# Kernel tuning notes

Hardware: AMD Instinct MI355X
Metric: run time of the kernel (lower is better)

The kernel has to match this reference:

```python
import jax, jax.numpy as jnp
import numpy as np

B, V = 4, 10242
N = B * V            # 40968 packed vertices
E_PER = 30720        # edges per mesh
HID = 128


def _bilinear_sample(fm, grid):
    """pytorch3d vert_align core: grid_sample(align_corners=True, bilinear).
    fm: [B,C,H,W], grid: [B,V,2] xy in [-1,1] -> [B,V,C]."""
    b_, c_, h_, w_ = fm.shape
    x = (grid[..., 0] + 1.0) * 0.5 * (w_ - 1)
    y = (grid[..., 1] + 1.0) * 0.5 * (h_ - 1)
    x0f, y0f = jnp.floor(x), jnp.floor(y)
    wx1, wy1 = x - x0f, y - y0f
    wx0, wy0 = 1.0 - wx1, 1.0 - wy1
    x0 = jnp.clip(x0f, 0, w_ - 1).astype(jnp.int32)
    x1 = jnp.clip(x0f + 1, 0, w_ - 1).astype(jnp.int32)
    y0 = jnp.clip(y0f, 0, h_ - 1).astype(jnp.int32)
    y1 = jnp.clip(y0f + 1, 0, h_ - 1).astype(jnp.int32)
    fmt = jnp.transpose(fm, (0, 2, 3, 1))  # [B,H,W,C]
    bi = jnp.arange(b_)[:, None]
    g = lambda yy, xx: fmt[bi, yy, xx]     # [B,V,C]
    return ((wy0 * wx0)[..., None] * g(y0, x0)
            + (wy0 * wx1)[..., None] * g(y0, x1)
            + (wy1 * wx0)[..., None] * g(y1, x0)
            + (wy1 * wx1)[..., None] * g(y1, x1))


def _graph_conv(x, edges, w0, b0, w1, b1):
    """pytorch3d GraphConv (undirected): W0 x_i + sum over both edge dirs of W1 x_j."""
    h0 = x @ w0 + b0
    h1 = x @ w1 + b1
    e0, e1 = edges[:, 0], edges[:, 1]
    agg = jnp.zeros_like(h0).at[e0].add(h1[e1]).at[e1].add(h1[e0])
    return h0 + agg


def setup_inputs() -> dict:
    key = jax.random.key(0)
    ks = jax.random.split(key, 20)
    s = 0.05
    # per-mesh edges, offset into packed index space
    e = jax.random.randint(ks[0], (B, E_PER, 2), 0, V)
    e = e + (jnp.arange(B) * V)[:, None, None]
    return {
        "feat1": jax.random.normal(ks[1], (B, 256, 56, 56), jnp.float32),
        "feat2": jax.random.normal(ks[2], (B, 512, 28, 28), jnp.float32),
        "feat3": jax.random.normal(ks[3], (B, 1024, 14, 14), jnp.float32),
        "feat4": jax.random.normal(ks[4], (B, 2048, 7, 7), jnp.float32),
        "aligned_verts": jax.random.uniform(ks[5], (B, V, 3), jnp.float32, -1.0, 1.0),
        "verts_packed": jax.random.normal(ks[6], (N, 3), jnp.float32),
        "image_enc": jax.random.normal(ks[7], (B, 256), jnp.float32),
        "edges": e.reshape(B * E_PER, 2).astype(jnp.int64),
        "bottleneck_w": jax.random.normal(ks[8], (3840, HID), jnp.float32) * s,
        "bottleneck_b": jnp.zeros((HID,), jnp.float32),
        "g0_w0": jax.random.normal(ks[9], (387, HID), jnp.float32) * s,
        "g0_b0": jnp.zeros((HID,), jnp.float32),
        "g0_w1": jax.random.normal(ks[10], (387, HID), jnp.float32) * s,
        "g0_b1": jnp.zeros((HID,), jnp.float32),
        "gw0": jax.random.normal(ks[11], (7, HID, HID), jnp.float32) * s,
        "gb0": jnp.zeros((7, HID), jnp.float32),
        "gw1": jax.random.normal(ks[12], (7, HID, HID), jnp.float32) * s,
        "gb1": jnp.zeros((7, HID), jnp.float32),
        "off_w": jax.random.normal(ks[13], (HID, 3), jnp.float32) * s,
        "off_b": jnp.zeros((3,), jnp.float32),
    }


def reference(feat1, feat2, feat3, feat4, aligned_verts, verts_packed, image_enc,
              edges, bottleneck_w, bottleneck_b, g0_w0, g0_b0, g0_w1, g0_b1,
              gw0, gb0, gw1, gb1, off_w, off_b):
    grid = aligned_verts[..., :2]  # vert_align uses xy only
    samp = jnp.concatenate([_bilinear_sample(f, grid)
                            for f in (feat1, feat2, feat3, feat4)], axis=-1)
    samp = samp.reshape(N, 3840)  # return_packed=True
    vfeat = jax.nn.relu(samp @ bottleneck_w + bottleneck_b)
    enc = jnp.repeat(image_enc, V, axis=0)  # repeat_interleave
    x = jnp.concatenate([vfeat, verts_packed, enc], axis=1)  # [N,387]
    x = jax.nn.relu(_graph_conv(x, edges, g0_w0, g0_b0, g0_w1, g0_b1))
    for i in range(7):
        x = jax.nn.relu(_graph_conv(x, edges, gw0[i], gb0[i], gw1[i], gb1[i]))
    return x @ off_w + off_b  # delta_v [N,3]
```

## Files before the change

kernel.cpp:

```cpp
#include <hip/hip_runtime.h>

static inline int ceil_div(int a, int b) { return (a + b - 1) / b; }

typedef __attribute__((ext_vector_type(8))) short short8;
typedef __attribute__((ext_vector_type(4))) float floatx4;

__device__ __forceinline__ unsigned short f2bf(float f) {
    unsigned int u = __float_as_uint(f);
    unsigned int r = (u + 0x7fffu + ((u >> 16) & 1u)) >> 16;
    return (unsigned short)r;
}
__device__ __forceinline__ float bf2f(unsigned short h) {
    return __uint_as_float(((unsigned int)h) << 16);
}

__global__ __launch_bounds__(1024) void scan1_k(const int* __restrict__ deg,
                                                int* __restrict__ excl,
                                                int* __restrict__ bsum, int Nv) {
    __shared__ int s[1024];
    int tid = threadIdx.x;
    int i = blockIdx.x * 1024 + tid;
    int v = (i < Nv) ? deg[i] : 0;
    s[tid] = v;
    __syncthreads();
    for (int off = 1; off < 1024; off <<= 1) {
        int t = (tid >= off) ? s[tid - off] : 0;
        __syncthreads();
        if (tid >= off) s[tid] += t;
        __syncthreads();
    }
    if (i < Nv) excl[i] = s[tid] - v;
    if (tid == 1023) bsum[blockIdx.x] = s[1023];
}

__global__ __launch_bounds__(64) void scan2_k(int* __restrict__ bsum, int nb) {
    __shared__ int s[64];
    int tid = threadIdx.x;
    int v = (tid < nb) ? bsum[tid] : 0;
    s[tid] = v;
    __syncthreads();
    for (int off = 1; off < 64; off <<= 1) {
        int t = (tid >= off) ? s[tid - off] : 0;
        __syncthreads();
        if (tid >= off) s[tid] += t;
        __syncthreads();
    }
    if (tid < nb) bsum[tid] = s[tid] - v;
}

__global__ __launch_bounds__(1024) void scan3_k(const int* __restrict__ excl,
                                                const int* __restrict__ bsum,
                                                const int* __restrict__ deg,
                                                int* __restrict__ rowptr,
                                                int* __restrict__ cursor, int Nv) {
    int i = blockIdx.x * 1024 + threadIdx.x;
    if (i < Nv) {
        int val = excl[i] + bsum[blockIdx.x];
        rowptr[i] = val;
        cursor[i] = val;
        if (i == Nv - 1) rowptr[Nv] = val + deg[i];
    }
}

__global__ __launch_bounds__(256) void fill_adj_k(const int* __restrict__ edges,
                                                  int* __restrict__ cursor,
                                                  int* __restrict__ adj, int E) {
    int e = blockIdx.x * blockDim.x + threadIdx.x;
    if (e < E) {
        int a = edges[2 * e], b = edges[2 * e + 1];
        adj[atomicAdd(&cursor[a], 1)] = b;
        adj[atomicAdd(&cursor[b], 1)] = a;
    }
}

__global__ __launch_bounds__(256) void fatpre_k(const int* __restrict__ edges,
                                                int* __restrict__ deg, int E, int nE,
                                                const float* __restrict__ g0w0,
                                                const float* __restrict__ g0w1,
                                                const float* __restrict__ gw0,
                                                const float* __restrict__ gw1,
                                                unsigned short* __restrict__ Wt,
                                                const float* __restrict__ enc,
                                                float* __restrict__ encp, int B_) {
    int bid = blockIdx.x;
    int tid = threadIdx.x;
    if (bid < nE) {
        int e = bid * 256 + tid;
        if (e < E) {
            atomicAdd(&deg[edges[2 * e]], 1);
            atomicAdd(&deg[edges[2 * e + 1]], 1);
        }
    } else if (bid < nE + 16) {
        int lh = bid - nE;
        int l = lh >> 1, h = lh & 1;
        const float* src;
        if (l == 0) src = h ? g0w1 : g0w0;
        else src = (h ? gw1 : gw0) + (size_t)(l - 1) * 16384;
        unsigned short* dst = Wt + (size_t)lh * 16384;
        for (int idx = tid; idx < 16384; idx += 256) {
            int n = idx >> 7, k = idx & 127;
            dst[n * 128 + k] = f2bf(src[k * 128 + n]);
        }
    } else {
        int b = bid - nE - 16;
        int sH = tid >> 7;
        int j = tid & 127;
        const float* w = sH ? g0w1 : g0w0;
        const float* eb = enc + b * 256;
        float acc = 0.f;
        for (int c = 0; c < 256; ++c) acc = fmaf(eb[c], w[(131 + c) * 128 + j], acc);
        encp[(sH * B_ + b) * 128 + j] = acc;
    }
}

__global__ __launch_bounds__(256) void proj_all_k(
    const float* __restrict__ fm1, const float* __restrict__ fm2,
    const float* __restrict__ fm3, const float* __restrict__ fm4,
    const float* __restrict__ bw, float* __restrict__ q1, float* __restrict__ q2,
    float* __restrict__ q3, float* __restrict__ q4, int B_) {
    __shared__ float Xs[32][64];
    __shared__ float Ws[32][128];
    int tid = threadIdx.x;

    int n1 = 49 * B_ * 4, n2 = 13 * B_ * 8, n3 = 4 * B_ * 16;
    int bid = blockIdx.x;
    const float* fm;
    const float* W;
    float* op;
    int C, HW, PT, idx;
    if (bid < n1) {
        fm = fm1; W = bw; op = q1; C = 256; HW = 3136; PT = 49; idx = bid;
    } else if (bid < n1 + n2) {
        fm = fm2; W = bw + 256 * 128; op = q2; C = 512; HW = 784; PT = 13; idx = bid - n1;
    } else if (bid < n1 + n2 + n3) {
        fm = fm3; W = bw + 768 * 128; op = q3; C = 1024; HW = 196; PT = 4; idx = bid - n1 - n2;
    } else {
        fm = fm4; W = bw + 1792 * 128; op = q4; C = 2048; HW = 49; PT = 1;
        idx = bid - n1 - n2 - n3;
    }
    int pt = idx % PT;
    int r2 = idx / PT;
    int b = r2 % B_;
    int zz = r2 / B_;
    int p0 = pt * 64;
    int c0 = zz * 64;
    int S = B_ * HW * 128;
    const float* fmb = fm + (size_t)b * C * HW;

    float acc[8][4];
#pragma unroll
    for (int i = 0; i < 8; i++)
#pragma unroll
        for (int j = 0; j < 4; j++) acc[i][j] = 0.f;

    bool vec_ok = ((HW & 3) == 0);
    for (int kc = c0; kc < c0 + 64; kc += 32) {
        {
            int p4 = (tid & 15) * 4;
            int k0 = tid >> 4;
#pragma unroll
            for (int kk = 0; kk < 32; kk += 16) {
                int k = k0 + kk;
                const float* src = fmb + (size_t)(kc + k) * HW + p0 + p4;
                float4 v;
                if (vec_ok && (p0 + p4 + 3 < HW)) {
                    v = *(const float4*)src;
                } else {
                    v.x = (p0 + p4 + 0 < HW) ? src[0] : 0.f;
                    v.y = (p0 + p4 + 1 < HW) ? src[1] : 0.f;
                    v.z = (p0 + p4 + 2 < HW) ? src[2] : 0.f;
                    v.w = (p0 + p4 + 3 < HW) ? src[3] : 0.f;
                }
                *(float4*)&Xs[k][p4] = v;
            }
        }
        {
            int j4 = (tid & 31) * 4;
            int k0 = tid >> 5;
#pragma unroll
            for (int kk = 0; kk < 32; kk += 8) {
                int k = k0 + kk;
                *(float4*)&Ws[k][j4] = *(const float4*)(W + (size_t)(kc + k) * 128 + j4);
            }
        }
        __syncthreads();
        int rb = (tid >> 5) * 8;
        int cb = (tid & 31) * 4;
#pragma unroll 8
        for (int k = 0; k < 32; ++k) {
            float xr[8], wc[4];
#pragma unroll
            for (int i = 0; i < 8; i++) xr[i] = Xs[k][rb + i];
#pragma unroll
            for (int j = 0; j < 4; j++) wc[j] = Ws[k][cb + j];
#pragma unroll
            for (int i = 0; i < 8; i++)
#pragma unroll
                for (int j = 0; j < 4; j++) acc[i][j] = fmaf(xr[i], wc[j], acc[i][j]);
        }
        __syncthreads();
    }
    int rb = (tid >> 5) * 8;
    int cb = (tid & 31) * 4;
    float* obase = op + (size_t)zz * S;
#pragma unroll
    for (int i = 0; i < 8; i++) {
        int p = p0 + rb + i;
        if (p < HW) {
            *(float4*)(obase + ((size_t)b * HW + p) * 128 + cb) =
                make_float4(acc[i][0], acc[i][1], acc[i][2], acc[i][3]);
        }
    }
}

__global__ __launch_bounds__(256) void reduce4_k(const float* __restrict__ q1,
                                                 const float* __restrict__ q2,
                                                 const float* __restrict__ q3,
                                                 const float* __restrict__ q4,
                                                 float* __restrict__ o1, float* __restrict__ o2,
                                                 float* __restrict__ o3, float* __restrict__ o4,
                                                 int S1, int S2, int S3, int S4) {
    int i = (blockIdx.x * 256 + threadIdx.x) * 4;
    const float* src;
    float* dst;
    int S, z, base;
    if (i < S1) {
        src = q1; dst = o1; S = S1; z = 4; base = i;
    } else if (i < S1 + S2) {
        src = q2; dst = o2; S = S2; z = 8; base = i - S1;
    } else if (i < S1 + S2 + S3) {
        src = q3; dst = o3; S = S3; z = 16; base = i - S1 - S2;
    } else if (i < S1 + S2 + S3 + S4) {
        src = q4; dst = o4; S = S4; z = 32; base = i - S1 - S2 - S3;
    } else {
        return;
    }
    float4 a = *(const float4*)(src + base);
    for (int zz = 1; zz < z; ++zz) {
        float4 b = *(const float4*)(src + (size_t)zz * S + base);
        a.x += b.x; a.y += b.y; a.z += b.z; a.w += b.w;
    }
    *(float4*)(dst + base) = a;
}

__device__ __forceinline__ float sample_level(const float* __restrict__ pp, int Hh, int Ww,
                                              float gx, float gy, int j) {
    float x = (gx + 1.f) * 0.5f * (float)(Ww - 1);
    float y = (gy + 1.f) * 0.5f * (float)(Hh - 1);
    float x0f = floorf(x), y0f = floorf(y);
    float wx1 = x - x0f, wy1 = y - y0f;
    float wx0 = 1.f - wx1, wy0 = 1.f - wy1;
    int x0 = (int)fminf(fmaxf(x0f, 0.f), (float)(Ww - 1));
    int x1 = (int)fminf(fmaxf(x0f + 1.f, 0.f), (float)(Ww - 1));
    int y0 = (int)fminf(fmaxf(y0f, 0.f), (float)(Hh - 1));
    int y1 = (int)fminf(fmaxf(y0f + 1.f, 0.f), (float)(Hh - 1));
    const float* r00 = pp + (size_t)(y0 * Ww + x0) * 128;
    const float* r01 = pp + (size_t)(y0 * Ww + x1) * 128;
    const float* r10 = pp + (size_t)(y1 * Ww + x0) * 128;
    const float* r11 = pp + (size_t)(y1 * Ww + x1) * 128;
    return wy0 * (wx0 * r00[j] + wx1 * r01[j]) + wy1 * (wx0 * r10[j] + wx1 * r11[j]);
}

__global__ __launch_bounds__(128) void sample_bottleneck_k(
    const float* __restrict__ av, const float* __restrict__ pp1, const float* __restrict__ pp2,
    const float* __restrict__ pp3, const float* __restrict__ pp4, const float* __restrict__ bb,
    const float* __restrict__ verts, const float* __restrict__ encp,
    const float* __restrict__ g0w0, const float* __restrict__ g0w1,
    const float* __restrict__ g0b0, const float* __restrict__ g0b1,
    unsigned short* __restrict__ X, unsigned short* __restrict__ H, int V_, int B_) {
    int n = blockIdx.x, j = threadIdx.x;
    int b = n / V_;
    float gx = av[(size_t)n * 3 + 0];
    float gy = av[(size_t)n * 3 + 1];
    float acc = bb[j];
    acc += sample_level(pp1 + (size_t)b * 3136 * 128, 56, 56, gx, gy, j);
    acc += sample_level(pp2 + (size_t)b * 784 * 128, 28, 28, gx, gy, j);
    acc += sample_level(pp3 + (size_t)b * 196 * 128, 14, 14, gx, gy, j);
    acc += sample_level(pp4 + (size_t)b * 49 * 128, 7, 7, gx, gy, j);
    X[(size_t)n * 128 + j] = f2bf(fmaxf(acc, 0.f));
    float v0 = verts[n * 3 + 0], v1 = verts[n * 3 + 1], v2 = verts[n * 3 + 2];
    float h0 = encp[(0 * B_ + b) * 128 + j] + g0b0[j] + v0 * g0w0[128 * 128 + j] +
               v1 * g0w0[129 * 128 + j] + v2 * g0w0[130 * 128 + j];
    float h1 = encp[(1 * B_ + b) * 128 + j] + g0b1[j] + v0 * g0w1[128 * 128 + j] +
               v1 * g0w1[129 * 128 + j] + v2 * g0w1[130 * 128 + j];
    H[(size_t)n * 256 + j] = f2bf(h0);
    H[(size_t)n * 256 + 128 + j] = f2bf(h1);
}

__global__ __launch_bounds__(256) void aggpre_k(const unsigned short* __restrict__ H,
                                                const int* __restrict__ rowptr,
                                                const int* __restrict__ adj,
                                                float* __restrict__ pre, int Nv) {
    int wave = threadIdx.x >> 6, lane = threadIdx.x & 63;
    int n = blockIdx.x * 4 + wave;
    if (n >= Nv) return;
    unsigned int u = *(const unsigned int*)(H + (size_t)n * 256 + 2 * lane);
    float a0 = bf2f((unsigned short)(u & 0xffff));
    float a1 = bf2f((unsigned short)(u >> 16));
    int s = rowptr[n], e = rowptr[n + 1];
    for (int t = s; t < e; t += 8) {
        int nb[8];
        unsigned int w[8];
#pragma unroll
        for (int q = 0; q < 8; ++q) {
            int idx = (t + q < e) ? (t + q) : (e - 1);
            nb[q] = adj[idx];
        }
#pragma unroll
        for (int q = 0; q < 8; ++q)
            w[q] = *(const unsigned int*)(H + (size_t)nb[q] * 256 + 128 + 2 * lane);
#pragma unroll
        for (int q = 0; q < 8; ++q) {
            if (t + q < e) {
                a0 += bf2f((unsigned short)(w[q] & 0xffff));
                a1 += bf2f((unsigned short)(w[q] >> 16));
            }
        }
    }
    pre[(size_t)n * 128 + 2 * lane] = a0;
    pre[(size_t)n * 128 + 2 * lane + 1] = a1;
}

__global__ __launch_bounds__(256) void agg_x_k(const unsigned short* __restrict__ X,
                                               const int* __restrict__ rowptr,
                                               const int* __restrict__ adj,
                                               unsigned short* __restrict__ Agg, int Nv) {
    int wave = threadIdx.x >> 6, lane = threadIdx.x & 63;
    int n = blockIdx.x * 4 + wave;
    if (n >= Nv) return;
    const unsigned int* Xu = (const unsigned int*)X;
    float a0 = 0.f, a1 = 0.f;
    int s = rowptr[n], e = rowptr[n + 1];
    for (int t = s; t < e; t += 8) {
        int nb[8];
        unsigned int w[8];
#pragma unroll
        for (int q = 0; q < 8; ++q) {
            int idx = (t + q < e) ? (t + q) : (e - 1);
            nb[q] = adj[idx];
        }
#pragma unroll
        for (int q = 0; q < 8; ++q) w[q] = Xu[(size_t)nb[q] * 64 + lane];
#pragma unroll
        for (int q = 0; q < 8; ++q) {
            if (t + q < e) {
                a0 += bf2f((unsigned short)(w[q] & 0xffff));
                a1 += bf2f((unsigned short)(w[q] >> 16));
            }
        }
    }
    unsigned int o = (unsigned int)f2bf(a0) | ((unsigned int)f2bf(a1) << 16);
    *(unsigned int*)(Agg + (size_t)n * 128 + 2 * lane) = o;
}

__global__ __launch_bounds__(256, 3) void gemm_dual_k(
    const unsigned short* __restrict__ Xin, const unsigned short* __restrict__ Agg,
    const unsigned short* __restrict__ Wt,
    const float* __restrict__ b0, const float* __restrict__ b1,
    const float* __restrict__ pre, const int* __restrict__ degv,
    unsigned short* __restrict__ Xout, int M) {
    __shared__ unsigned short wlds[16384];
    __shared__ unsigned short cs[64 * 72];
    __shared__ float bS[128];

    int tid = threadIdx.x;
    int m0 = blockIdx.x * 128;
    int yb = blockIdx.y;

    int wave = tid >> 6, lane = tid & 63;
    int row16 = lane & 15;
    int quad = lane >> 4;
    int wrow = wave * 16;

    short8 axT[2][4], agT[2][4];
    int dgT[2][4];
    {
        int g = min(m0 + wrow + row16, M - 1);
#pragma unroll
        for (int ks = 0; ks < 4; ++ks) {
            int koff = ks * 32 + quad * 8;
            axT[0][ks] = *(const short8*)(Xin + (size_t)g * 128 + koff);
            agT[0][ks] = *(const short8*)(Agg + (size_t)g * 128 + koff);
        }
#pragma unroll
        for (int rr = 0; rr < 4; ++rr)
            dgT[0][rr] = degv[min(m0 + wrow + quad * 4 + rr, M - 1)];
    }

    if (tid < 64) {
        bS[tid] = b0 ? b0[yb * 64 + tid] : 0.f;
        bS[64 + tid] = b1 ? b1[yb * 64 + tid] : 0.f;
    }

    const unsigned short* W0h = Wt + (size_t)yb * 64 * 128;
    const unsigned short* W1h = Wt + 16384 + (size_t)yb * 64 * 128;
#pragma unroll
    for (int l = 0; l < 8; ++l) {
        int idx = tid + l * 256;
        int half = idx >> 10;
        int r = (idx >> 4) & 63;
        int c16 = idx & 15;
        int sw = (c16 ^ (r & 15)) * 8;
        const unsigned short* src = (half ? W1h : W0h) + r * 128 + c16 * 8;
        *(short8*)&wlds[half * 8192 + r * 128 + sw] = *(const short8*)src;
    }
    __syncthreads();

    {
        int g = min(m0 + 64 + wrow + row16, M - 1);
#pragma unroll
        for (int ks = 0; ks < 4; ++ks) {
            int koff = ks * 32 + quad * 8;
            axT[1][ks] = *(const short8*)(Xin + (size_t)g * 128 + koff);
            agT[1][ks] = *(const short8*)(Agg + (size_t)g * 128 + koff);
        }
#pragma unroll
        for (int rr = 0; rr < 4; ++rr)
            dgT[1][rr] = degv[min(m0 + 64 + wrow + quad * 4 + rr, M - 1)];
    }

#pragma unroll
    for (int t = 0; t < 2; ++t) {
        int mT = m0 + t * 64;
        floatx4 acc[4];
#pragma unroll
        for (int j = 0; j < 4; j++) acc[j] = (floatx4){0.f, 0.f, 0.f, 0.f};

#pragma unroll
        for (int ks = 0; ks < 4; ++ks) {
            int c = ks * 4 + quad;
#pragma unroll
            for (int nt = 0; nt < 4; ++nt) {
                int wr = nt * 16 + row16;
                short8 bw0 = *(short8*)&wlds[wr * 128 + ((c ^ row16) * 8)];
                short8 bw1 = *(short8*)&wlds[8192 + wr * 128 + ((c ^ row16) * 8)];
                acc[nt] = __builtin_amdgcn_mfma_f32_16x16x32_bf16(axT[t][ks], bw0, acc[nt], 0, 0, 0);
                acc[nt] = __builtin_amdgcn_mfma_f32_16x16x32_bf16(agT[t][ks], bw1, acc[nt], 0, 0, 0);
            }
        }

#pragma unroll
        for (int nt = 0; nt < 4; ++nt) {
            int colh = nt * 16 + row16;
            int colg = yb * 64 + colh;
            float bc0 = bS[colh];
            float bc1 = bS[64 + colh];
#pragma unroll
            for (int rr = 0; rr < 4; ++rr) {
                int row = wrow + quad * 4 + rr;
                int gm = mT + row;
                float v = acc[nt][rr] + bc0 + (float)dgT[t][rr] * bc1;
                if (pre && gm < M) v += pre[(size_t)gm * 128 + colg];
                cs[row * 72 + colh] = f2bf(fmaxf(v, 0.f));
            }
        }
        __syncthreads();

        {
            int r = tid >> 2;
            int cq = (tid & 3) * 16;
            int gm = mT + r;
            if (gm < M) {
                unsigned short* dst = Xout + (size_t)gm * 128 + yb * 64 + cq;
                *(short8*)dst = *(short8*)&cs[r * 72 + cq];
                *(short8*)(dst + 8) = *(short8*)&cs[r * 72 + cq + 8];
            }
        }
        __syncthreads();
    }
}

__global__ __launch_bounds__(256) void head_k(const unsigned short* __restrict__ X,
                                              const float* __restrict__ off_w,
                                              const float* __restrict__ off_b,
                                              float* __restrict__ out, int Nv) {
    int wave = threadIdx.x >> 6, lane = threadIdx.x & 63;
    int n = blockIdx.x * 4 + wave;
    if (n >= Nv) return;
    unsigned int u = *(const unsigned int*)(X + (size_t)n * 128 + 2 * lane);
    float x0 = bf2f((unsigned short)(u & 0xffff));
    float x1 = bf2f((unsigned short)(u >> 16));
    int c0 = 2 * lane, c1 = 2 * lane + 1;
    float p0 = x0 * off_w[c0 * 3 + 0] + x1 * off_w[c1 * 3 + 0];
    float p1 = x0 * off_w[c0 * 3 + 1] + x1 * off_w[c1 * 3 + 1];
    float p2 = x0 * off_w[c0 * 3 + 2] + x1 * off_w[c1 * 3 + 2];
#pragma unroll
    for (int m = 1; m < 64; m <<= 1) {
        p0 += __shfl_xor(p0, m);
        p1 += __shfl_xor(p1, m);
        p2 += __shfl_xor(p2, m);
    }
    if (lane == 0) {
        out[n * 3 + 0] = p0 + off_b[0];
        out[n * 3 + 1] = p1 + off_b[1];
        out[n * 3 + 2] = p2 + off_b[2];
    }
}

extern "C" void kernel_launch(void* const* d_in, const int* in_sizes, int n_in, void* d_out,
                              int out_size, void* d_ws, size_t ws_size, hipStream_t stream) {
    const float* feat1 = (const float*)d_in[0];
    const float* feat2 = (const float*)d_in[1];
    const float* feat3 = (const float*)d_in[2];
    const float* feat4 = (const float*)d_in[3];
    const float* av = (const float*)d_in[4];
    const float* verts = (const float*)d_in[5];
    const float* image_enc = (const float*)d_in[6];
    const int* edges = (const int*)d_in[7];
    const float* bw = (const float*)d_in[8];
    const float* bb = (const float*)d_in[9];
    const float* g0w0 = (const float*)d_in[10];
    const float* g0b0 = (const float*)d_in[11];
    const float* g0w1 = (const float*)d_in[12];
    const float* g0b1 = (const float*)d_in[13];
    const float* gw0 = (const float*)d_in[14];
    const float* gb0 = (const float*)d_in[15];
    const float* gw1 = (const float*)d_in[16];
    const float* gb1 = (const float*)d_in[17];
    const float* off_w = (const float*)d_in[18];
    const float* off_b = (const float*)d_in[19];

    int B_ = in_sizes[6] / 256;
    int N_ = in_sizes[5] / 3;
    int V_ = N_ / B_;
    int E_ = in_sizes[7] / 2;

    char* wsb = (char*)d_ws;
    size_t off = 0;
    auto alloc = [&](size_t bytes) -> void* {
        void* p = (void*)(wsb + off);
        off += (bytes + 255) & ~(size_t)255;
        return p;
    };
    int S1 = B_ * 3136 * 128;
    int S2 = B_ * 784 * 128;
    int S3 = B_ * 196 * 128;
    int S4 = B_ * 49 * 128;
    float* pp1 = (float*)alloc((size_t)S1 * 4);
    float* pp2 = (float*)alloc((size_t)S2 * 4);
    float* pp3 = (float*)alloc((size_t)S3 * 4);
    float* pp4 = (float*)alloc((size_t)S4 * 4);
    float* q1 = (float*)alloc((size_t)4 * S1 * 4);
    float* q2 = (float*)alloc((size_t)8 * S2 * 4);
    float* q3 = (float*)alloc((size_t)16 * S3 * 4);
    float* q4 = (float*)alloc((size_t)32 * S4 * 4);
    unsigned short* XA = (unsigned short*)alloc((size_t)N_ * 128 * 2);
    unsigned short* XB = (unsigned short*)alloc((size_t)N_ * 128 * 2);
    unsigned short* AggB = (unsigned short*)alloc((size_t)N_ * 128 * 2);
    unsigned short* Hb = (unsigned short*)alloc((size_t)N_ * 256 * 2);
    float* pre = (float*)alloc((size_t)N_ * 128 * 4);
    unsigned short* Wt = (unsigned short*)alloc((size_t)8 * 2 * 128 * 128 * 2);
    float* encp = (float*)alloc((size_t)2 * B_ * 128 * 4);
    int* deg = (int*)alloc((size_t)(N_ + 1) * 4);
    int* rowptr = (int*)alloc((size_t)(N_ + 1) * 4);
    int* cursor = (int*)alloc((size_t)N_ * 4);
    int* excl = (int*)alloc((size_t)N_ * 4);
    int* bsum = (int*)alloc((size_t)64 * 4);
    int* adj = (int*)alloc((size_t)2 * E_ * 4);

    hipMemsetAsync(deg, 0, (N_ + 1) * sizeof(int), stream);

    int nE = ceil_div(E_, 256);
    fatpre_k<<<nE + 16 + B_, 256, 0, stream>>>(edges, deg, E_, nE, g0w0, g0w1, gw0, gw1, Wt,
                                               image_enc, encp, B_);

    int nb = ceil_div(N_, 1024);
    scan1_k<<<nb, 1024, 0, stream>>>(deg, excl, bsum, N_);
    scan2_k<<<1, 64, 0, stream>>>(bsum, nb);
    scan3_k<<<nb, 1024, 0, stream>>>(excl, bsum, deg, rowptr, cursor, N_);
    fill_adj_k<<<ceil_div(E_, 256), 256, 0, stream>>>(edges, cursor, adj, E_);

    int nproj = 49 * B_ * 4 + 13 * B_ * 8 + 4 * B_ * 16 + 1 * B_ * 32;
    proj_all_k<<<nproj, 256, 0, stream>>>(feat1, feat2, feat3, feat4, bw, q1, q2, q3, q4, B_);
    int tot4 = (S1 + S2 + S3 + S4) / 4;
    reduce4_k<<<ceil_div(tot4, 256), 256, 0, stream>>>(q1, q2, q3, q4, pp1, pp2, pp3, pp4, S1,
                                                       S2, S3, S4);

    sample_bottleneck_k<<<N_, 128, 0, stream>>>(av, pp1, pp2, pp3, pp4, bb, verts, encp, g0w0,
                                                g0w1, g0b0, g0b1, XA, Hb, V_, B_);

    aggpre_k<<<ceil_div(N_, 4), 256, 0, stream>>>(Hb, rowptr, adj, pre, N_);

    int agrid = ceil_div(N_, 4);
    dim3 ggrid(ceil_div(N_, 128), 2);
    agg_x_k<<<agrid, 256, 0, stream>>>(XA, rowptr, adj, AggB, N_);
    gemm_dual_k<<<ggrid, 256, 0, stream>>>(XA, AggB, Wt, nullptr, nullptr, pre, deg, XB, N_);
    unsigned short* Xc = XB;
    unsigned short* Xn = XA;
    for (int i = 0; i < 7; ++i) {
        agg_x_k<<<agrid, 256, 0, stream>>>(Xc, rowptr, adj, AggB, N_);
        gemm_dual_k<<<ggrid, 256, 0, stream>>>(Xc, AggB, Wt + (size_t)(i + 1) * 32768,
                                               gb0 + i * 128, gb1 + i * 128, nullptr, deg, Xn,
                                               N_);
        unsigned short* t = Xc;
        Xc = Xn;
        Xn = t;
    }
    head_k<<<ceil_div(N_, 4), 256, 0, stream>>>(Xc, off_w, off_b, (float*)d_out, N_);
}
```

Baseline: 493.5 us.

## Fuse neighbor aggregation into dual GEMM per graph-conv layer

Replaces the separate agg_x_k and gemm_dual_k launches with one kernel per layer. Each block gathers and sums neighbor features for 64 rows into LDS, using a wave-level CSR walk that flushes each row's sum when its edge range ends. It then runs both MFMA products over all 128 output columns using a 64KB LDS weight tile. This removes the Agg buffer round trip through global memory and half the launches. In exchange, LDS use per block is larger (occupancy hint drops to 2), and each wave walks its rows' edges serially, which can leave waves unevenly loaded.

```diff
diff --git a/kernel.cpp b/kernel.cpp
--- a/kernel.cpp
+++ b/kernel.cpp
@@ -321,152 +321,145 @@
     pre[(size_t)n * 128 + 2 * lane + 1] = a1;
 }
 
-__global__ __launch_bounds__(256) void agg_x_k(const unsigned short* __restrict__ X,
-                                               const int* __restrict__ rowptr,
-                                               const int* __restrict__ adj,
-                                               unsigned short* __restrict__ Agg, int Nv) {
-    int wave = threadIdx.x >> 6, lane = threadIdx.x & 63;
-    int n = blockIdx.x * 4 + wave;
-    if (n >= Nv) return;
-    const unsigned int* Xu = (const unsigned int*)X;
-    float a0 = 0.f, a1 = 0.f;
-    int s = rowptr[n], e = rowptr[n + 1];
-    for (int t = s; t < e; t += 8) {
-        int nb[8];
-        unsigned int w[8];
-#pragma unroll
-        for (int q = 0; q < 8; ++q) {
-            int idx = (t + q < e) ? (t + q) : (e - 1);
-            nb[q] = adj[idx];
-        }
-#pragma unroll
-        for (int q = 0; q < 8; ++q) w[q] = Xu[(size_t)nb[q] * 64 + lane];
-#pragma unroll
-        for (int q = 0; q < 8; ++q) {
-            if (t + q < e) {
-                a0 += bf2f((unsigned short)(w[q] & 0xffff));
-                a1 += bf2f((unsigned short)(w[q] >> 16));
-            }
-        }
-    }
-    unsigned int o = (unsigned int)f2bf(a0) | ((unsigned int)f2bf(a1) << 16);
-    *(unsigned int*)(Agg + (size_t)n * 128 + 2 * lane) = o;
-}
-
-__global__ __launch_bounds__(256, 3) void gemm_dual_k(
-    const unsigned short* __restrict__ Xin, const unsigned short* __restrict__ Agg,
+__global__ __launch_bounds__(256, 2) void layer_fused_k(
+    const unsigned short* __restrict__ Xin, const int* __restrict__ rowptr,
+    const int* __restrict__ adj,
     const unsigned short* __restrict__ Wt,
     const float* __restrict__ b0, const float* __restrict__ b1,
     const float* __restrict__ pre, const int* __restrict__ degv,
     unsigned short* __restrict__ Xout, int M) {
-    __shared__ unsigned short wlds[16384];
-    __shared__ unsigned short cs[64 * 72];
-    __shared__ float bS[128];
+    __shared__ unsigned short wlds[32768];
+    __shared__ unsigned short aggs[8192];
 
     int tid = threadIdx.x;
-    int m0 = blockIdx.x * 128;
-    int yb = blockIdx.y;
-
+    int m0 = blockIdx.x * 64;
     int wave = tid >> 6, lane = tid & 63;
     int row16 = lane & 15;
     int quad = lane >> 4;
-    int wrow = wave * 16;
-
-    short8 axT[2][4], agT[2][4];
-    int dgT[2][4];
+
+    int gbase = m0 + wave * 16;
+    int rend_l = rowptr[min(gbase + 1 + row16, M)];
+    int sW = rowptr[min(gbase, M)];
+    int eW = __shfl(rend_l, 15);
+
+    short8 axT[4];
     {
-        int g = min(m0 + wrow + row16, M - 1);
-#pragma unroll
-        for (int ks = 0; ks < 4; ++ks) {
-            int koff = ks * 32 + quad * 8;
-            axT[0][ks] = *(const short8*)(Xin + (size_t)g * 128 + koff);
-            agT[0][ks] = *(const short8*)(Agg + (size_t)g * 128 + koff);
-        }
-#pragma unroll
-        for (int rr = 0; rr < 4; ++rr)
-            dgT[0][rr] = degv[min(m0 + wrow + quad * 4 + rr, M - 1)];
-    }
-
-    if (tid < 64) {
-        bS[tid] = b0 ? b0[yb * 64 + tid] : 0.f;
-        bS[64 + tid] = b1 ? b1[yb * 64 + tid] : 0.f;
-    }
-
-    const unsigned short* W0h = Wt + (size_t)yb * 64 * 128;
-    const unsigned short* W1h = Wt + 16384 + (size_t)yb * 64 * 128;
-#pragma unroll
-    for (int l = 0; l < 8; ++l) {
+        int g = min(m0 + wave * 16 + row16, M - 1);
+#pragma unroll
+        for (int ks = 0; ks < 4; ++ks)
+            axT[ks] = *(const short8*)(Xin + (size_t)g * 128 + ks * 32 + quad * 8);
+    }
+    int dgT[4];
+#pragma unroll
+    for (int rr = 0; rr < 4; ++rr)
+        dgT[rr] = degv[min(m0 + wave * 16 + quad * 4 + rr, M - 1)];
+    float bc0[8], bc1[8];
+#pragma unroll
+    for (int nt = 0; nt < 8; ++nt) {
+        int colg = nt * 16 + row16;
+        bc0[nt] = b0 ? b0[colg] : 0.f;
+        bc1[nt] = b1 ? b1[colg] : 0.f;
+    }
+
+#pragma unroll
+    for (int l = 0; l < 16; ++l) {
         int idx = tid + l * 256;
-        int half = idx >> 10;
-        int r = (idx >> 4) & 63;
+        int half = idx >> 11;
+        int n = (idx >> 4) & 127;
         int c16 = idx & 15;
-        int sw = (c16 ^ (r & 15)) * 8;
-        const unsigned short* src = (half ? W1h : W0h) + r * 128 + c16 * 8;
-        *(short8*)&wlds[half * 8192 + r * 128 + sw] = *(const short8*)src;
+        int sw = (c16 ^ (n & 15)) * 8;
+        *(short8*)&wlds[half * 16384 + n * 128 + sw] =
+            *(const short8*)(Wt + (size_t)half * 16384 + n * 128 + c16 * 8);
+    }
+
+    {
+        const unsigned int* Xu = (const unsigned int*)Xin;
+        float a0 = 0.f, a1 = 0.f;
+        int r = 0;
+        int nextEnd = __shfl(rend_l, 0);
+        auto flush = [&](int rloc, float v0, float v1) {
+            unsigned int o = (unsigned int)f2bf(v0) | ((unsigned int)f2bf(v1) << 16);
+            *(unsigned int*)&aggs[(wave * 16 + rloc) * 128 + (((lane >> 2) ^ rloc) * 8) +
+                                  (lane & 3) * 2] = o;
+        };
+        for (int t = sW; t < eW; t += 8) {
+            int nb[8];
+            unsigned int w[8];
+#pragma unroll
+            for (int q = 0; q < 8; ++q) {
+                int idx = (t + q < eW) ? (t + q) : (eW - 1);
+                nb[q] = adj[idx];
+            }
+#pragma unroll
+            for (int q = 0; q < 8; ++q) w[q] = Xu[(size_t)nb[q] * 64 + lane];
+#pragma unroll
+            for (int q = 0; q < 8; ++q) {
+                int pos = t + q;
+                if (pos < eW) {
+                    while (pos >= nextEnd) {
+                        flush(r, a0, a1);
+                        a0 = 0.f;
+                        a1 = 0.f;
+                        ++r;
+                        nextEnd = __shfl(rend_l, r);
+                    }
+                    a0 += bf2f((unsigned short)(w[q] & 0xffff));
+                    a1 += bf2f((unsigned short)(w[q] >> 16));
+                }
+            }
+        }
+        while (r < 16) {
+            flush(r, a0, a1);
+            a0 = 0.f;
+            a1 = 0.f;
+            ++r;
+        }
     }
     __syncthreads();
 
+    floatx4 acc[8];
+#pragma unroll
+    for (int j = 0; j < 8; ++j) acc[j] = (floatx4){0.f, 0.f, 0.f, 0.f};
+#pragma unroll
+    for (int ks = 0; ks < 4; ++ks) {
+        int c = ks * 4 + quad;
+        short8 aAg = *(short8*)&aggs[(wave * 16 + row16) * 128 + ((c ^ row16) * 8)];
+#pragma unroll
+        for (int nt = 0; nt < 8; ++nt) {
+            int wr = nt * 16 + row16;
+            short8 bw0 = *(short8*)&wlds[wr * 128 + ((c ^ row16) * 8)];
+            short8 bw1 = *(short8*)&wlds[16384 + wr * 128 + ((c ^ row16) * 8)];
+            acc[nt] = __builtin_amdgcn_mfma_f32_16x16x32_bf16(axT[ks], bw0, acc[nt], 0, 0, 0);
+            acc[nt] = __builtin_amdgcn_mfma_f32_16x16x32_bf16(aAg, bw1, acc[nt], 0, 0, 0);
+        }
+    }
+
+#pragma unroll
+    for (int nt = 0; nt < 8; ++nt) {
+#pragma unroll
+        for (int rr = 0; rr < 4; ++rr) {
+            int row = wave * 16 + quad * 4 + rr;
+            int gm = m0 + row;
+            int colh = nt * 16 + row16;
+            float v = acc[nt][rr] + bc0[nt] + (float)dgT[rr] * bc1[nt];
+            if (pre && gm < M) v += pre[(size_t)gm * 128 + colh];
+            int ch = colh >> 3;
+            aggs[row * 128 + ((ch ^ (row & 15)) * 8) + (colh & 7)] = f2bf(fmaxf(v, 0.f));
+        }
+    }
+    __syncthreads();
+
     {
-        int g = min(m0 + 64 + wrow + row16, M - 1);
-#pragma unroll
-        for (int ks = 0; ks < 4; ++ks) {
-            int koff = ks * 32 + quad * 8;
-            axT[1][ks] = *(const short8*)(Xin + (size_t)g * 128 + koff);
-            agT[1][ks] = *(const short8*)(Agg + (size_t)g * 128 + koff);
-        }
-#pragma unroll
-        for (int rr = 0; rr < 4; ++rr)
-            dgT[1][rr] = degv[min(m0 + 64 + wrow + quad * 4 + rr, M - 1)];
-    }
-
-#pragma unroll
-    for (int t = 0; t < 2; ++t) {
-        int mT = m0 + t * 64;
-        floatx4 acc[4];
-#pragma unroll
-        for (int j = 0; j < 4; j++) acc[j] = (floatx4){0.f, 0.f, 0.f, 0.f};
-
-#pragma unroll
-        for (int ks = 0; ks < 4; ++ks) {
-            int c = ks * 4 + quad;
-#pragma unroll
-            for (int nt = 0; nt < 4; ++nt) {
-                int wr = nt * 16 + row16;
-                short8 bw0 = *(short8*)&wlds[wr * 128 + ((c ^ row16) * 8)];
-                short8 bw1 = *(short8*)&wlds[8192 + wr * 128 + ((c ^ row16) * 8)];
-                acc[nt] = __builtin_amdgcn_mfma_f32_16x16x32_bf16(axT[t][ks], bw0, acc[nt], 0, 0, 0);
-                acc[nt] = __builtin_amdgcn_mfma_f32_16x16x32_bf16(agT[t][ks], bw1, acc[nt], 0, 0, 0);
+        int r = tid >> 2;
+        int gm = m0 + r;
+        if (gm < M) {
+            unsigned short* dst = Xout + (size_t)gm * 128 + (tid & 3) * 32;
+#pragma unroll
+            for (int cc = 0; cc < 4; ++cc) {
+                int c = (tid & 3) * 4 + cc;
+                *(short8*)(dst + cc * 8) = *(short8*)&aggs[r * 128 + ((c ^ (r & 15)) * 8)];
             }
         }
-
-#pragma unroll
-        for (int nt = 0; nt < 4; ++nt) {
-            int colh = nt * 16 + row16;
-            int colg = yb * 64 + colh;
-            float bc0 = bS[colh];
-            float bc1 = bS[64 + colh];
-#pragma unroll
-            for (int rr = 0; rr < 4; ++rr) {
-                int row = wrow + quad * 4 + rr;
-                int gm = mT + row;
-                float v = acc[nt][rr] + bc0 + (float)dgT[t][rr] * bc1;
-                if (pre && gm < M) v += pre[(size_t)gm * 128 + colg];
-                cs[row * 72 + colh] = f2bf(fmaxf(v, 0.f));
-            }
-        }
-        __syncthreads();
-
-        {
-            int r = tid >> 2;
-            int cq = (tid & 3) * 16;
-            int gm = mT + r;
-            if (gm < M) {
-                unsigned short* dst = Xout + (size_t)gm * 128 + yb * 64 + cq;
-                *(short8*)dst = *(short8*)&cs[r * 72 + cq];
-                *(short8*)(dst + 8) = *(short8*)&cs[r * 72 + cq + 8];
-            }
-        }
-        __syncthreads();
     }
 }
 
@@ -546,7 +539,6 @@
     float* q4 = (float*)alloc((size_t)32 * S4 * 4);
     unsigned short* XA = (unsigned short*)alloc((size_t)N_ * 128 * 2);
     unsigned short* XB = (unsigned short*)alloc((size_t)N_ * 128 * 2);
-    unsigned short* AggB = (unsigned short*)alloc((size_t)N_ * 128 * 2);
     unsigned short* Hb = (unsigned short*)alloc((size_t)N_ * 256 * 2);
     float* pre = (float*)alloc((size_t)N_ * 128 * 4);
     unsigned short* Wt = (unsigned short*)alloc((size_t)8 * 2 * 128 * 128 * 2);
@@ -581,17 +573,15 @@
 
     aggpre_k<<<ceil_div(N_, 4), 256, 0, stream>>>(Hb, rowptr, adj, pre, N_);
 
-    int agrid = ceil_div(N_, 4);
-    dim3 ggrid(ceil_div(N_, 128), 2);
-    agg_x_k<<<agrid, 256, 0, stream>>>(XA, rowptr, adj, AggB, N_);
-    gemm_dual_k<<<ggrid, 256, 0, stream>>>(XA, AggB, Wt, nullptr, nullptr, pre, deg, XB, N_);
+    dim3 fgrid(ceil_div(N_, 64));
+    layer_fused_k<<<fgrid, 256, 0, stream>>>(XA, rowptr, adj, Wt, nullptr, nullptr, pre, deg,
+                                             XB, N_);
     unsigned short* Xc = XB;
     unsigned short* Xn = XA;
     for (int i = 0; i < 7; ++i) {
-        agg_x_k<<<agrid, 256, 0, stream>>>(Xc, rowptr, adj, AggB, N_);
-        gemm_dual_k<<<ggrid, 256, 0, stream>>>(Xc, AggB, Wt + (size_t)(i + 1) * 32768,
-                                               gb0 + i * 128, gb1 + i * 128, nullptr, deg, Xn,
-                                               N_);
+        layer_fused_k<<<fgrid, 256, 0, stream>>>(Xc, rowptr, adj, Wt + (size_t)(i + 1) * 32768,
+                                                 gb0 + i * 128, gb1 + i * 128, nullptr, deg, Xn,
+                                                 N_);
         unsigned short* t = Xc;
         Xc = Xn;
         Xn = t;
```

After: 588.8 us. +19.3%, slower.

## Use bf16 MFMA for feature projection and XCD-aware vertex mapping in aggregation

Applied to the files above, without the earlier changes.

The fp32 FMA tiled GEMM in the feature-map projection is replaced by bf16 MFMA 16x16x32. The bottleneck weight is pre-transposed to bf16 in the prologue kernel and staged in LDS with an XOR swizzle. Separately, the aggregation kernels remap block indices so that each XCD pair handles a single mesh, which should improve L2 locality for neighbor gathers. This lowers projection precision to bf16 and uses uncoalesced per-lane feature loads.

```diff
diff --git a/kernel.cpp b/kernel.cpp
--- a/kernel.cpp
+++ b/kernel.cpp
@@ -80,6 +80,8 @@
                                                 const float* __restrict__ gw0,
                                                 const float* __restrict__ gw1,
                                                 unsigned short* __restrict__ Wt,
+                                                const float* __restrict__ bw,
+                                                unsigned short* __restrict__ bwT,
                                                 const float* __restrict__ enc,
                                                 float* __restrict__ encp, int B_) {
     int bid = blockIdx.x;
@@ -101,8 +103,15 @@
             int n = idx >> 7, k = idx & 127;
             dst[n * 128 + k] = f2bf(src[k * 128 + n]);
         }
+    } else if (bid < nE + 46) {
+        int blk = bid - nE - 16;
+        for (int idx = tid; idx < 16384; idx += 256) {
+            int n = idx >> 7, kk = idx & 127;
+            bwT[(size_t)n * 3840 + blk * 128 + kk] =
+                f2bf(bw[(size_t)(blk * 128 + kk) * 128 + n]);
+        }
     } else {
-        int b = bid - nE - 16;
+        int b = bid - nE - 46;
         int sH = tid >> 7;
         int j = tid & 127;
         const float* w = sH ? g0w1 : g0w0;
@@ -116,99 +125,81 @@
 __global__ __launch_bounds__(256) void proj_all_k(
     const float* __restrict__ fm1, const float* __restrict__ fm2,
     const float* __restrict__ fm3, const float* __restrict__ fm4,
-    const float* __restrict__ bw, float* __restrict__ q1, float* __restrict__ q2,
+    const unsigned short* __restrict__ bwT, float* __restrict__ q1, float* __restrict__ q2,
     float* __restrict__ q3, float* __restrict__ q4, int B_) {
-    __shared__ float Xs[32][64];
-    __shared__ float Ws[32][128];
+    __shared__ unsigned short wlds[8192];
+
     int tid = threadIdx.x;
-
     int n1 = 49 * B_ * 4, n2 = 13 * B_ * 8, n3 = 4 * B_ * 16;
     int bid = blockIdx.x;
     const float* fm;
-    const float* W;
     float* op;
-    int C, HW, PT, idx;
+    int C, HW, PT, idx, koff;
     if (bid < n1) {
-        fm = fm1; W = bw; op = q1; C = 256; HW = 3136; PT = 49; idx = bid;
+        fm = fm1; op = q1; C = 256; HW = 3136; PT = 49; idx = bid; koff = 0;
     } else if (bid < n1 + n2) {
-        fm = fm2; W = bw + 256 * 128; op = q2; C = 512; HW = 784; PT = 13; idx = bid - n1;
+        fm = fm2; op = q2; C = 512; HW = 784; PT = 13; idx = bid - n1; koff = 256;
     } else if (bid < n1 + n2 + n3) {
-        fm = fm3; W = bw + 768 * 128; op = q3; C = 1024; HW = 196; PT = 4; idx = bid - n1 - n2;
+        fm = fm3; op = q3; C = 1024; HW = 196; PT = 4; idx = bid - n1 - n2; koff = 768;
     } else {
-        fm = fm4; W = bw + 1792 * 128; op = q4; C = 2048; HW = 49; PT = 1;
-        idx = bid - n1 - n2 - n3;
+        fm = fm4; op = q4; C = 2048; HW = 49; PT = 1; idx = bid - n1 - n2 - n3; koff = 1792;
     }
     int pt = idx % PT;
     int r2 = idx / PT;
     int b = r2 % B_;
     int zz = r2 / B_;
     int p0 = pt * 64;
-    int c0 = zz * 64;
     int S = B_ * HW * 128;
     const float* fmb = fm + (size_t)b * C * HW;
-
-    float acc[8][4];
-#pragma unroll
-    for (int i = 0; i < 8; i++)
-#pragma unroll
-        for (int j = 0; j < 4; j++) acc[i][j] = 0.f;
-
-    bool vec_ok = ((HW & 3) == 0);
-    for (int kc = c0; kc < c0 + 64; kc += 32) {
-        {
-            int p4 = (tid & 15) * 4;
-            int k0 = tid >> 4;
-#pragma unroll
-            for (int kk = 0; kk < 32; kk += 16) {
-                int k = k0 + kk;
-                const float* src = fmb + (size_t)(kc + k) * HW + p0 + p4;
-                float4 v;
-                if (vec_ok && (p0 + p4 + 3 < HW)) {
-                    v = *(const float4*)src;
-                } else {
-                    v.x = (p0 + p4 + 0 < HW) ? src[0] : 0.f;
-                    v.y = (p0 + p4 + 1 < HW) ? src[1] : 0.f;
-                    v.z = (p0 + p4 + 2 < HW) ? src[2] : 0.f;
-                    v.w = (p0 + p4 + 3 < HW) ? src[3] : 0.f;
-                }
-                *(float4*)&Xs[k][p4] = v;
-            }
-        }
-        {
-            int j4 = (tid & 31) * 4;
-            int k0 = tid >> 5;
-#pragma unroll
-            for (int kk = 0; kk < 32; kk += 8) {
-                int k = k0 + kk;
-                *(float4*)&Ws[k][j4] = *(const float4*)(W + (size_t)(kc + k) * 128 + j4);
-            }
-        }
-        __syncthreads();
-        int rb = (tid >> 5) * 8;
-        int cb = (tid & 31) * 4;
-#pragma unroll 8
-        for (int k = 0; k < 32; ++k) {
-            float xr[8], wc[4];
-#pragma unroll
-            for (int i = 0; i < 8; i++) xr[i] = Xs[k][rb + i];
-#pragma unroll
-            for (int j = 0; j < 4; j++) wc[j] = Ws[k][cb + j];
-#pragma unroll
-            for (int i = 0; i < 8; i++)
-#pragma unroll
-                for (int j = 0; j < 4; j++) acc[i][j] = fmaf(xr[i], wc[j], acc[i][j]);
-        }
-        __syncthreads();
-    }
-    int rb = (tid >> 5) * 8;
-    int cb = (tid & 31) * 4;
-    float* obase = op + (size_t)zz * S;
-#pragma unroll
-    for (int i = 0; i < 8; i++) {
-        int p = p0 + rb + i;
-        if (p < HW) {
-            *(float4*)(obase + ((size_t)b * HW + p) * 128 + cb) =
-                make_float4(acc[i][0], acc[i][1], acc[i][2], acc[i][3]);
+    int kcf = zz * 64;
+    int kcw = koff + kcf;
+
+#pragma unroll
+    for (int l = 0; l < 4; ++l) {
+        int i2 = tid + l * 256;
+        int n = i2 >> 3, c16 = i2 & 7;
+        *(short8*)&wlds[n * 64 + ((c16 ^ (n & 7)) * 8)] =
+            *(const short8*)(bwT + (size_t)n * 3840 + kcw + c16 * 8);
+    }
+
+    int wave = tid >> 6, lane = tid & 63;
+    int row16 = lane & 15, quad = lane >> 4;
+    int p = p0 + wave * 16 + row16;
+    bool pok = (p < HW);
+    int pc = pok ? p : 0;
+    short8 ax[2];
+#pragma unroll
+    for (int ks = 0; ks < 2; ++ks) {
+#pragma unroll
+        for (int j = 0; j < 8; ++j) {
+            float v = pok ? fmb[(size_t)(kcf + ks * 32 + quad * 8 + j) * HW + pc] : 0.f;
+            ax[ks][j] = (short)f2bf(v);
+        }
+    }
+    __syncthreads();
+
+    floatx4 acc[8];
+#pragma unroll
+    for (int j = 0; j < 8; ++j) acc[j] = (floatx4){0.f, 0.f, 0.f, 0.f};
+#pragma unroll
+    for (int ks = 0; ks < 2; ++ks) {
+        int c = ks * 4 + quad;
+#pragma unroll
+        for (int nt = 0; nt < 8; ++nt) {
+            int wr = nt * 16 + row16;
+            short8 bwf = *(short8*)&wlds[wr * 64 + ((c ^ (wr & 7)) * 8)];
+            acc[nt] = __builtin_amdgcn_mfma_f32_16x16x32_bf16(ax[ks], bwf, acc[nt], 0, 0, 0);
+        }
+    }
+
+    float* obase = op + (size_t)zz * S + (size_t)b * HW * 128;
+#pragma unroll
+    for (int nt = 0; nt < 8; ++nt) {
+        int colg = nt * 16 + row16;
+#pragma unroll
+        for (int rr = 0; rr < 4; ++rr) {
+            int pr = p0 + wave * 16 + quad * 4 + rr;
+            if (pr < HW) obase[(size_t)pr * 128 + colg] = acc[nt][rr];
         }
     }
 }
@@ -287,13 +278,26 @@
     H[(size_t)n * 256 + 128 + j] = f2bf(h1);
 }
 
+__device__ __forceinline__ int xcd_vertex(int bid, int wave, int V_, int B_, int Nv) {
+    if (B_ == 4) {
+        int xcd = bid & 7;
+        int lb = (bid >> 3) * 2 + (xcd & 1);
+        int lv = lb * 4 + wave;
+        if (lv >= V_) return -1;
+        return (xcd >> 1) * V_ + lv;
+    }
+    int n = bid * 4 + wave;
+    return (n < Nv) ? n : -1;
+}
+
 __global__ __launch_bounds__(256) void aggpre_k(const unsigned short* __restrict__ H,
                                                 const int* __restrict__ rowptr,
                                                 const int* __restrict__ adj,
-                                                float* __restrict__ pre, int Nv) {
+                                                float* __restrict__ pre, int Nv, int V_,
+                                                int B_) {
     int wave = threadIdx.x >> 6, lane = threadIdx.x & 63;
-    int n = blockIdx.x * 4 + wave;
-    if (n >= Nv) return;
+    int n = xcd_vertex(blockIdx.x, wave, V_, B_, Nv);
+    if (n < 0) return;
     unsigned int u = *(const unsigned int*)(H + (size_t)n * 256 + 2 * lane);
     float a0 = bf2f((unsigned short)(u & 0xffff));
     float a1 = bf2f((unsigned short)(u >> 16));
@@ -324,10 +328,11 @@
 __global__ __launch_bounds__(256) void agg_x_k(const unsigned short* __restrict__ X,
                                                const int* __restrict__ rowptr,
                                                const int* __restrict__ adj,
-                                               unsigned short* __restrict__ Agg, int Nv) {
+                                               unsigned short* __restrict__ Agg, int Nv,
+                                               int V_, int B_) {
     int wave = threadIdx.x >> 6, lane = threadIdx.x & 63;
-    int n = blockIdx.x * 4 + wave;
-    if (n >= Nv) return;
+    int n = xcd_vertex(blockIdx.x, wave, V_, B_, Nv);
+    if (n < 0) return;
     const unsigned int* Xu = (const unsigned int*)X;
     float a0 = 0.f, a1 = 0.f;
     int s = rowptr[n], e = rowptr[n + 1];
@@ -550,6 +555,7 @@
     unsigned short* Hb = (unsigned short*)alloc((size_t)N_ * 256 * 2);
     float* pre = (float*)alloc((size_t)N_ * 128 * 4);
     unsigned short* Wt = (unsigned short*)alloc((size_t)8 * 2 * 128 * 128 * 2);
+    unsigned short* bwT = (unsigned short*)alloc((size_t)128 * 3840 * 2);
     float* encp = (float*)alloc((size_t)2 * B_ * 128 * 4);
     int* deg = (int*)alloc((size_t)(N_ + 1) * 4);
     int* rowptr = (int*)alloc((size_t)(N_ + 1) * 4);
@@ -561,8 +567,8 @@
     hipMemsetAsync(deg, 0, (N_ + 1) * sizeof(int), stream);
 
     int nE = ceil_div(E_, 256);
-    fatpre_k<<<nE + 16 + B_, 256, 0, stream>>>(edges, deg, E_, nE, g0w0, g0w1, gw0, gw1, Wt,
-                                               image_enc, encp, B_);
+    fatpre_k<<<nE + 46 + B_, 256, 0, stream>>>(edges, deg, E_, nE, g0w0, g0w1, gw0, gw1, Wt,
+                                               bw, bwT, image_enc, encp, B_);
 
     int nb = ceil_div(N_, 1024);
     scan1_k<<<nb, 1024, 0, stream>>>(deg, excl, bsum, N_);
@@ -571,7 +577,7 @@
     fill_adj_k<<<ceil_div(E_, 256), 256, 0, stream>>>(edges, cursor, adj, E_);
 
     int nproj = 49 * B_ * 4 + 13 * B_ * 8 + 4 * B_ * 16 + 1 * B_ * 32;
-    proj_all_k<<<nproj, 256, 0, stream>>>(feat1, feat2, feat3, feat4, bw, q1, q2, q3, q4, B_);
+    proj_all_k<<<nproj, 256, 0, stream>>>(feat1, feat2, feat3, feat4, bwT, q1, q2, q3, q4, B_);
     int tot4 = (S1 + S2 + S3 + S4) / 4;
     reduce4_k<<<ceil_div(tot4, 256), 256, 0, stream>>>(q1, q2, q3, q4, pp1, pp2, pp3, pp4, S1,
                                                        S2, S3, S4);
@@ -579,16 +585,17 @@
     sample_bottleneck_k<<<N_, 128, 0, stream>>>(av, pp1, pp2, pp3, pp4, bb, verts, encp, g0w0,
                                                 g0w1, g0b0, g0b1, XA, Hb, V_, B_);
 
-    aggpre_k<<<ceil_div(N_, 4), 256, 0, stream>>>(Hb, rowptr, adj, pre, N_);
-
-    int agrid = ceil_div(N_, 4);
+    int agrid = (B_ == 4) ? 8 * ceil_div(ceil_div(V_, 4), 2) : ceil_div(N_, 4);
+
+    aggpre_k<<<agrid, 256, 0, stream>>>(Hb, rowptr, adj, pre, N_, V_, B_);
+
     dim3 ggrid(ceil_div(N_, 128), 2);
-    agg_x_k<<<agrid, 256, 0, stream>>>(XA, rowptr, adj, AggB, N_);
+    agg_x_k<<<agrid, 256, 0, stream>>>(XA, rowptr, adj, AggB, N_, V_, B_);
     gemm_dual_k<<<ggrid, 256, 0, stream>>>(XA, AggB, Wt, nullptr, nullptr, pre, deg, XB, N_);
     unsigned short* Xc = XB;
     unsigned short* Xn = XA;
     for (int i = 0; i < 7; ++i) {
-        agg_x_k<<<agrid, 256, 0, stream>>>(Xc, rowptr, adj, AggB, N_);
+        agg_x_k<<<agrid, 256, 0, stream>>>(Xc, rowptr, adj, AggB, N_, V_, B_);
         gemm_dual_k<<<ggrid, 256, 0, stream>>>(Xc, AggB, Wt + (size_t)(i + 1) * 32768,
                                                gb0 + i * 128, gb1 + i * 128, nullptr, deg, Xn,
                                                N_);
```

Result: faster. 476.4 us (-3.5%).
